# Optimization experiments

Hardware: AMD Instinct MI355X
Metric: run time of the kernel (lower is better)

The kernel has to match this reference:

```python
import jax, jax.numpy as jnp
import numpy as np

VOCAB, EMBED, BLOCK, HEADS, LAYERS = 96, 192, 128, 6, 6
HS = EMBED // HEADS  # 32
B, T = 256, 128
EPS = 1e-5


def layer_norm(x, g, b):
    m = jnp.mean(x, axis=-1, keepdims=True)
    v = jnp.mean(jnp.square(x - m), axis=-1, keepdims=True)
    return (x - m) * jax.lax.rsqrt(v + EPS) * g + b


def setup_inputs() -> dict:
    key = jax.random.key(0)
    ks = jax.random.split(key, 20)
    s = 0.02
    return {
        "index": jax.random.randint(ks[0], (B, T), 0, VOCAB),
        "targets": jax.random.randint(ks[1], (B, T), 0, VOCAB),
        "tok_emb": jax.random.normal(ks[2], (VOCAB, EMBED), jnp.float32) * s,
        "pos_emb": jax.random.normal(ks[3], (BLOCK, EMBED), jnp.float32) * s,
        "ln1_g": jnp.ones((LAYERS, EMBED), jnp.float32),
        "ln1_b": jnp.zeros((LAYERS, EMBED), jnp.float32),
        "ln2_g": jnp.ones((LAYERS, EMBED), jnp.float32),
        "ln2_b": jnp.zeros((LAYERS, EMBED), jnp.float32),
        "Wq": jax.random.normal(ks[4], (LAYERS, HEADS, EMBED, HS), jnp.float32) * s,
        "Wk": jax.random.normal(ks[5], (LAYERS, HEADS, EMBED, HS), jnp.float32) * s,
        "Wv": jax.random.normal(ks[6], (LAYERS, HEADS, EMBED, HS), jnp.float32) * s,
        "W1": jax.random.normal(ks[7], (LAYERS, EMBED, 4 * EMBED), jnp.float32) * s,
        "b1": jnp.zeros((LAYERS, 4 * EMBED), jnp.float32),
        "W2": jax.random.normal(ks[8], (LAYERS, 4 * EMBED, EMBED), jnp.float32) * s,
        "b2": jnp.zeros((LAYERS, EMBED), jnp.float32),
        "fn_g": jnp.ones((EMBED,), jnp.float32),
        "fn_b": jnp.zeros((EMBED,), jnp.float32),
        "Wf": jax.random.normal(ks[9], (EMBED, VOCAB), jnp.float32) * s,
        "bf": jnp.zeros((VOCAB,), jnp.float32),
    }


def reference(index, targets, tok_emb, pos_emb, ln1_g, ln1_b, ln2_g, ln2_b,
              Wq, Wk, Wv, W1, b1, W2, b2, fn_g, fn_b, Wf, bf):
    t = index.shape[1]
    x = tok_emb[index] + pos_emb[:t]                      # [B,T,E]
    causal = jnp.tril(jnp.ones((t, t), bool))             # [T,T]
    for l in range(LAYERS):
        n1 = layer_norm(x, ln1_g[l], ln1_b[l])
        # --- per-head attention, computed but (faithfully) unused by the block ---
        q = jnp.einsum('bte,hes->bhts', n1, Wq[l])
        k = jnp.einsum('bte,hes->bhts', n1, Wk[l])
        v = jnp.einsum('bte,hes->bhts', n1, Wv[l])
        w = jnp.einsum('bhts,bhus->bhtu', q, k) * (EMBED ** -0.5)  # note: scaled by embed, as in source
        w = jnp.where(causal, w, -jnp.inf)
        wei = jax.nn.softmax(w, axis=-1)
        _attn_out = jnp.einsum('bhtu,bhus->bhts', wei, v)  # dead in original forward
        # --- actual block output: FFN on ln2(ln1(x)), no residual ---
        n2 = layer_norm(n1, ln2_g[l], ln2_b[l])
        h = jnp.maximum(jnp.einsum('bte,ef->btf', n2, W1[l]) + b1[l], 0.0)
        x = jnp.einsum('btf,fe->bte', h, W2[l]) + b2[l]
    x = layer_norm(x, fn_g, fn_b)
    logits = jnp.einsum('bte,ev->btv', x, Wf) + bf        # [B,T,V]
    pred = logits.reshape(-1, VOCAB)                      # [B*T,V]
    tgt = targets.reshape(-1)
    logp = jax.nn.log_softmax(pred, axis=-1)
    loss = -jnp.mean(jnp.take_along_axis(logp, tgt[:, None], axis=1)[:, 0])
    return pred, loss
```

## Files before the change

kernel.cpp:

```cpp
#include <hip/hip_runtime.h>

typedef __attribute__((ext_vector_type(4))) float f32x4;
typedef __attribute__((ext_vector_type(8))) short short8;
typedef unsigned short ushort_t;
typedef unsigned int uint_t;

#define R_  32768
#define L_  6
#define EPS_ 1e-5f

#define NW_ 884736

__device__ __forceinline__ ushort_t f2bf(float f) {
    uint_t i = __builtin_bit_cast(uint_t, f);
    uint_t r = (i + 0x7fffu + ((i >> 16) & 1u)) >> 16;
    return (ushort_t)r;
}
__device__ __forceinline__ uint_t cvtpk(float a, float b) {
    uint_t r;
    asm("v_cvt_pk_bf16_f32 %0, %1, %2" : "=v"(r) : "v"(a), "v"(b));
    return r;
}

__global__ void wconv_k(const float* __restrict__ W1, const float* __restrict__ W2,
                        const float* __restrict__ Wf,
                        ushort_t* __restrict__ w1s, ushort_t* __restrict__ w2s,
                        ushort_t* __restrict__ wfr)
{
    int i = blockIdx.x * 256 + threadIdx.x;
    if (i < NW_) {
        int j = i & 7, li = (i >> 3) & 63, q = i >> 9;
        int kc = q % 6; q /= 6;
        int ft = q % 6; q /= 6;
        int wv = q & 3; q >>= 2;
        int half = q & 1; int l = q >> 1;
        int f = half * 384 + wv * 96 + ft * 16 + (li & 15);
        int k = kc * 32 + ((li >> 4) << 3) + j;
        w1s[i] = f2bf(W1[((size_t)l * 192 + k) * 768 + f]);
        return;
    }
    i -= NW_;
    if (i < NW_) {
        int j = i & 7, li = (i >> 3) & 63, q = i >> 9;
        int kc2 = q % 12; q /= 12;
        int ei = q % 3; q /= 3;
        int wv = q & 3; q >>= 2;
        int half = q & 1; int l = q >> 1;
        int e = (wv + 4 * ei) * 16 + (li & 15);
        int k = half * 384 + kc2 * 32 + ((li >> 4) << 3) + j;
        w2s[i] = f2bf(W2[((size_t)l * 768 + k) * 192 + e]);
        return;
    }
    i -= NW_;
    if (i < 36 * 512) {
        int j = i & 7, li = (i >> 3) & 63, q = i >> 9;
        int kc = q % 6, vt = q / 6;
        int v = vt * 16 + (li & 15);
        int k = kc * 32 + ((li >> 4) << 3) + j;
        wfr[i] = f2bf(Wf[(size_t)k * 96 + v]);
    }
}

__global__ __launch_bounds__(256, 2) void net_k(
    const int* __restrict__ idxp, const int* __restrict__ tgp,
    const float* __restrict__ tok, const float* __restrict__ pos,
    const float* __restrict__ ln1g, const float* __restrict__ ln1b,
    const float* __restrict__ ln2g, const float* __restrict__ ln2b,
    const float* __restrict__ b1g, const float* __restrict__ b2g,
    const float* __restrict__ fng, const float* __restrict__ fnb,
    const float* __restrict__ bfb,
    const ushort_t* __restrict__ w1s, const ushort_t* __restrict__ w2s,
    const ushort_t* __restrict__ wfr,
    float* __restrict__ pred, float* __restrict__ partial)
{
    __shared__ __align__(16) ushort_t xb[6 * 4 * 512];
    __shared__ __align__(16) ushort_t hbl[12 * 4 * 512];
    __shared__ __align__(16) float lnS1[64][4], lnQ1[64][4];
    __shared__ __align__(16) float lnS2[64][4], lnQ2[64][4];
    __shared__ float lsred[4];

    const int tid = threadIdx.x, lane = tid & 63, w = tid >> 6;
    const int c = lane & 15, g = lane >> 4;
    const int row0 = blockIdx.x * 64;

    f32x4 xac[3][4];

#pragma unroll
    for (int rg = 0; rg < 4; ++rg) {
        int row = row0 + rg * 16 + c;
        int id = idxp[row];
        int tt = row & 127;
#pragma unroll
        for (int i = 0; i < 3; ++i) {
            int e0 = (w + 4 * i) * 16 + g * 4;
            float4 a = *(const float4*)(tok + (size_t)id * 192 + e0);
            float4 b = *(const float4*)(pos + (size_t)tt * 192 + e0);
            xac[i][rg][0] = a.x + b.x; xac[i][rg][1] = a.y + b.y;
            xac[i][rg][2] = a.z + b.z; xac[i][rg][3] = a.w + b.w;
        }
    }

#pragma unroll 1
    for (int l = 0; l < L_; ++l) {
#pragma unroll
        for (int rg = 0; rg < 4; ++rg) {
            float s = 0.f, sq = 0.f;
#pragma unroll
            for (int i = 0; i < 3; ++i)
#pragma unroll
                for (int r = 0; r < 4; ++r) { float v = xac[i][rg][r]; s += v; sq += v * v; }
            s += __shfl_xor(s, 16); sq += __shfl_xor(sq, 16);
            s += __shfl_xor(s, 32); sq += __shfl_xor(sq, 32);
            if (g == 0) { lnS1[rg * 16 + c][w] = s; lnQ1[rg * 16 + c][w] = sq; }
        }
        __syncthreads();
#pragma unroll
        for (int rg = 0; rg < 4; ++rg) {
            float4 S = *(const float4*)lnS1[rg * 16 + c];
            float4 Q = *(const float4*)lnQ1[rg * 16 + c];
            float mu = (S.x + S.y + S.z + S.w) * (1.f / 192.f);
            float var = (Q.x + Q.y + Q.z + Q.w) * (1.f / 192.f) - mu * mu;
            float ri = rsqrtf(var + EPS_);
            float s2 = 0.f, q2 = 0.f;
#pragma unroll
            for (int i = 0; i < 3; ++i) {
                int e0 = (w + 4 * i) * 16 + g * 4;
                float4 gg = *(const float4*)(ln1g + l * 192 + e0);
                float4 bb = *(const float4*)(ln1b + l * 192 + e0);
                float n0 = (xac[i][rg][0] - mu) * ri * gg.x + bb.x;
                float n1 = (xac[i][rg][1] - mu) * ri * gg.y + bb.y;
                float n2 = (xac[i][rg][2] - mu) * ri * gg.z + bb.z;
                float n3 = (xac[i][rg][3] - mu) * ri * gg.w + bb.w;
                xac[i][rg][0] = n0; xac[i][rg][1] = n1; xac[i][rg][2] = n2; xac[i][rg][3] = n3;
                s2 += n0 + n1 + n2 + n3;
                q2 += n0 * n0 + n1 * n1 + n2 * n2 + n3 * n3;
            }
            s2 += __shfl_xor(s2, 16); q2 += __shfl_xor(q2, 16);
            s2 += __shfl_xor(s2, 32); q2 += __shfl_xor(q2, 32);
            if (g == 0) { lnS2[rg * 16 + c][w] = s2; lnQ2[rg * 16 + c][w] = q2; }
        }
        __syncthreads();
#pragma unroll
        for (int rg = 0; rg < 4; ++rg) {
            float4 S = *(const float4*)lnS2[rg * 16 + c];
            float4 Q = *(const float4*)lnQ2[rg * 16 + c];
            float mu = (S.x + S.y + S.z + S.w) * (1.f / 192.f);
            float var = (Q.x + Q.y + Q.z + Q.w) * (1.f / 192.f) - mu * mu;
            float ri = rsqrtf(var + EPS_);
#pragma unroll
            for (int i = 0; i < 3; ++i) {
                int et = w + 4 * i;
                int e0 = et * 16 + g * 4;
                float4 gg = *(const float4*)(ln2g + l * 192 + e0);
                float4 bb = *(const float4*)(ln2b + l * 192 + e0);
                float y0 = (xac[i][rg][0] - mu) * ri * gg.x + bb.x;
                float y1 = (xac[i][rg][1] - mu) * ri * gg.y + bb.y;
                float y2 = (xac[i][rg][2] - mu) * ri * gg.z + bb.z;
                float y3 = (xac[i][rg][3] - mu) * ri * gg.w + bb.w;
                uint_t d0 = cvtpk(y0, y1), d1 = cvtpk(y2, y3);
                int kc = et >> 1, floc = ((et & 1) << 4) + g * 4;
                int us = (kc * 4 + rg) * 512 + ((floc >> 3) * 16 + c) * 8 + (floc & 7);
                *(uint2*)(xb + us) = make_uint2(d0, d1);
                float4 b2v = *(const float4*)(b2g + l * 192 + e0);
                xac[i][rg][0] = b2v.x; xac[i][rg][1] = b2v.y;
                xac[i][rg][2] = b2v.z; xac[i][rg][3] = b2v.w;
            }
        }
        __syncthreads();

#pragma unroll 1
        for (int half = 0; half < 2; ++half) {
            const ushort_t* w1p = w1s + ((size_t)((l * 2 + half) * 4 + w) * 36) * 512 + lane * 8;
#pragma unroll
            for (int fth = 0; fth < 2; ++fth) {
                short8 wa[18];
#pragma unroll
                for (int q = 0; q < 18; ++q) wa[q] = *(const short8*)(w1p + (fth * 18 + q) * 512);
                float4 bbv[3];
#pragma unroll
                for (int f3 = 0; f3 < 3; ++f3)
                    bbv[f3] = *(const float4*)(b1g + l * 768 + half * 384 + w * 96 + (fth * 3 + f3) * 16 + g * 4);
#pragma unroll
                for (int rg = 0; rg < 4; ++rg) {
                    short8 xbf[6];
#pragma unroll
                    for (int kc = 0; kc < 6; ++kc)
                        xbf[kc] = *(const short8*)(xb + (kc * 4 + rg) * 512 + lane * 8);
#pragma unroll
                    for (int f3 = 0; f3 < 3; ++f3) {
                        f32x4 acc;
                        acc[0] = bbv[f3].x; acc[1] = bbv[f3].y;
                        acc[2] = bbv[f3].z; acc[3] = bbv[f3].w;
                        __builtin_amdgcn_s_setprio(1);
#pragma unroll
                        for (int kc = 0; kc < 6; ++kc)
                            acc = __builtin_amdgcn_mfma_f32_16x16x32_bf16(wa[f3 * 6 + kc], xbf[kc], acc, 0, 0, 0);
                        __builtin_amdgcn_s_setprio(0);
                        float y0 = fmaxf(acc[0], 0.f);
                        float y1 = fmaxf(acc[1], 0.f);
                        float y2 = fmaxf(acc[2], 0.f);
                        float y3 = fmaxf(acc[3], 0.f);
                        uint_t d0 = cvtpk(y0, y1), d1 = cvtpk(y2, y3);
                        int ft = fth * 3 + f3;
                        int kc2 = w * 3 + (ft >> 1);
                        int floc = ((ft & 1) << 4) + g * 4;
                        int us = (kc2 * 4 + rg) * 512 + ((floc >> 3) * 16 + c) * 8 + (floc & 7);
                        *(uint2*)(hbl + us) = make_uint2(d0, d1);
                    }
                }
            }
            __syncthreads();

            const ushort_t* w2p = w2s + ((size_t)((l * 2 + half) * 4 + w) * 36) * 512 + lane * 8;
#pragma unroll
            for (int kh = 0; kh < 2; ++kh) {
                short8 wr[18];
#pragma unroll
                for (int ei = 0; ei < 3; ++ei)
#pragma unroll
                    for (int k6 = 0; k6 < 6; ++k6)
                        wr[ei * 6 + k6] = *(const short8*)(w2p + (ei * 12 + kh * 6 + k6) * 512);
#pragma unroll
                for (int rg = 0; rg < 4; ++rg) {
                    short8 hbf[6];
#pragma unroll
                    for (int k6 = 0; k6 < 6; ++k6)
                        hbf[k6] = *(const short8*)(hbl + ((kh * 6 + k6) * 4 + rg) * 512 + lane * 8);
                    __builtin_amdgcn_s_setprio(1);
#pragma unroll
                    for (int ei = 0; ei < 3; ++ei)
#pragma unroll
                        for (int k6 = 0; k6 < 6; ++k6)
                            xac[ei][rg] = __builtin_amdgcn_mfma_f32_16x16x32_bf16(wr[ei * 6 + k6], hbf[k6], xac[ei][rg], 0, 0, 0);
                    __builtin_amdgcn_s_setprio(0);
                }
            }
            if (half == 0) __syncthreads();
        }
    }

#pragma unroll
    for (int rg = 0; rg < 4; ++rg) {
        float s = 0.f, sq = 0.f;
#pragma unroll
        for (int i = 0; i < 3; ++i)
#pragma unroll
            for (int r = 0; r < 4; ++r) { float v = xac[i][rg][r]; s += v; sq += v * v; }
        s += __shfl_xor(s, 16); sq += __shfl_xor(sq, 16);
        s += __shfl_xor(s, 32); sq += __shfl_xor(sq, 32);
        if (g == 0) { lnS1[rg * 16 + c][w] = s; lnQ1[rg * 16 + c][w] = sq; }
    }
    __syncthreads();
#pragma unroll
    for (int rg = 0; rg < 4; ++rg) {
        float4 S = *(const float4*)lnS1[rg * 16 + c];
        float4 Q = *(const float4*)lnQ1[rg * 16 + c];
        float mu = (S.x + S.y + S.z + S.w) * (1.f / 192.f);
        float var = (Q.x + Q.y + Q.z + Q.w) * (1.f / 192.f) - mu * mu;
        float ri = rsqrtf(var + EPS_);
#pragma unroll
        for (int i = 0; i < 3; ++i) {
            int et = w + 4 * i;
            int e0 = et * 16 + g * 4;
            float4 gg = *(const float4*)(fng + e0);
            float4 bb = *(const float4*)(fnb + e0);
            float y0 = (xac[i][rg][0] - mu) * ri * gg.x + bb.x;
            float y1 = (xac[i][rg][1] - mu) * ri * gg.y + bb.y;
            float y2 = (xac[i][rg][2] - mu) * ri * gg.z + bb.z;
            float y3 = (xac[i][rg][3] - mu) * ri * gg.w + bb.w;
            uint_t d0 = cvtpk(y0, y1), d1 = cvtpk(y2, y3);
            int kc = et >> 1, floc = ((et & 1) << 4) + g * 4;
            int us = (kc * 4 + rg) * 512 + ((floc >> 3) * 16 + c) * 8 + (floc & 7);
            *(uint2*)(xb + us) = make_uint2(d0, d1);
        }
    }
    __syncthreads();

    short8 wfh[36];
    {
        const ushort_t* wfp = wfr + lane * 8;
#pragma unroll
        for (int q = 0; q < 36; ++q) wfh[q] = *(const short8*)(wfp + q * 512);
    }
    short8 xbf[6];
#pragma unroll
    for (int kc = 0; kc < 6; ++kc)
        xbf[kc] = *(const short8*)(xb + (kc * 4 + w) * 512 + lane * 8);
    f32x4 av[6] = {};
    __builtin_amdgcn_s_setprio(1);
#pragma unroll
    for (int vt = 0; vt < 6; ++vt)
#pragma unroll
        for (int kc = 0; kc < 6; ++kc)
            av[vt] = __builtin_amdgcn_mfma_f32_16x16x32_bf16(wfh[vt * 6 + kc], xbf[kc], av[vt], 0, 0, 0);
    __builtin_amdgcn_s_setprio(0);

    float vv[6][4];
#pragma unroll
    for (int vt = 0; vt < 6; ++vt) {
        float4 bb = *(const float4*)(bfb + vt * 16 + g * 4);
        vv[vt][0] = av[vt][0] + bb.x;
        vv[vt][1] = av[vt][1] + bb.y;
        vv[vt][2] = av[vt][2] + bb.z;
        vv[vt][3] = av[vt][3] + bb.w;
    }
    float mx = -1e30f;
#pragma unroll
    for (int vt = 0; vt < 6; ++vt)
#pragma unroll
        for (int r = 0; r < 4; ++r) mx = fmaxf(mx, vv[vt][r]);
    mx = fmaxf(mx, __shfl_xor(mx, 16));
    mx = fmaxf(mx, __shfl_xor(mx, 32));
    float se = 0.f;
#pragma unroll
    for (int vt = 0; vt < 6; ++vt)
#pragma unroll
        for (int r = 0; r < 4; ++r) se += expf(vv[vt][r] - mx);
    se += __shfl_xor(se, 16);
    se += __shfl_xor(se, 32);
    float lse = logf(se) + mx;
    int myrow = row0 + w * 16 + c;
    int tgt = tgp[myrow];
    float lsum = 0.f;
#pragma unroll
    for (int vt = 0; vt < 6; ++vt)
#pragma unroll
        for (int r = 0; r < 4; ++r)
            if (tgt == vt * 16 + g * 4 + r) lsum += lse - vv[vt][r];
#pragma unroll
    for (int vt = 0; vt < 6; ++vt) {
        float4 o;
        o.x = vv[vt][0]; o.y = vv[vt][1]; o.z = vv[vt][2]; o.w = vv[vt][3];
        *(float4*)(pred + (size_t)myrow * 96 + vt * 16 + g * 4) = o;
    }
#pragma unroll
    for (int m = 1; m < 64; m <<= 1) lsum += __shfl_xor(lsum, m);
    if (lane == 0) lsred[w] = lsum;
    __syncthreads();
    if (tid == 0) partial[blockIdx.x] = lsred[0] + lsred[1] + lsred[2] + lsred[3];
}

__global__ void lossred_k(const float* __restrict__ partial, float* __restrict__ out)
{
    __shared__ double sd[256];
    int t = threadIdx.x;
    sd[t] = (double)partial[t] + (double)partial[t + 256];
    __syncthreads();
    for (int s = 128; s > 0; s >>= 1) {
        if (t < s) sd[t] += sd[t + s];
        __syncthreads();
    }
    if (t == 0) out[0] = (float)(sd[0] / (double)R_);
}

extern "C" void kernel_launch(void* const* d_in, const int* in_sizes, int n_in,
                              void* d_out, int out_size, void* d_ws, size_t ws_size,
                              hipStream_t stream)
{
    (void)in_sizes; (void)n_in; (void)out_size; (void)ws_size;
    const int*   index   = (const int*)  d_in[0];
    const int*   targets = (const int*)  d_in[1];
    const float* tok     = (const float*)d_in[2];
    const float* pos     = (const float*)d_in[3];
    const float* ln1g    = (const float*)d_in[4];
    const float* ln1b    = (const float*)d_in[5];
    const float* ln2g    = (const float*)d_in[6];
    const float* ln2b    = (const float*)d_in[7];
    const float* W1      = (const float*)d_in[11];
    const float* b1      = (const float*)d_in[12];
    const float* W2      = (const float*)d_in[13];
    const float* b2      = (const float*)d_in[14];
    const float* fng     = (const float*)d_in[15];
    const float* fnb     = (const float*)d_in[16];
    const float* Wf      = (const float*)d_in[17];
    const float* bfv     = (const float*)d_in[18];

    ushort_t* w1s = (ushort_t*)d_ws;
    ushort_t* w2s = w1s + NW_;
    ushort_t* wfr = w2s + NW_;
    float* partial = (float*)(wfr + 36 * 512);
    float* pred  = (float*)d_out;
    float* lossp = pred + (size_t)R_ * 96;

    const int nconv = 2 * NW_ + 36 * 512;
    wconv_k<<<nconv / 256, 256, 0, stream>>>(W1, W2, Wf, w1s, w2s, wfr);
    net_k<<<512, 256, 0, stream>>>(index, targets, tok, pos, ln1g, ln1b, ln2g, ln2b,
                                   b1, b2, fng, fnb, bfv, w1s, w2s, wfr, pred, partial);
    lossred_k<<<1, 256, 0, stream>>>(partial, lossp);
}
```

Baseline: 148.6 us.

## Split FFN hidden dim into quarters to shrink LDS and raise occupancy

The FFN hidden dimension is now processed in four chunks of 192 instead of two halves of 384. This halves the hidden-activation LDS buffer and cuts per-wave weight register arrays, so launch bounds can ask for 3 blocks per SM instead of 2. The W1/W2 pre-swizzle layout is rewritten to match, and the final projection loads its weights in two groups to lower register pressure. The cost is twice as many barriers per layer and smaller weight tiles between syncs, which gives less latency hiding per block.

```diff
diff --git a/kernel.cpp b/kernel.cpp
--- a/kernel.cpp
+++ b/kernel.cpp
@@ -31,10 +31,10 @@
     if (i < NW_) {
         int j = i & 7, li = (i >> 3) & 63, q = i >> 9;
         int kc = q % 6; q /= 6;
-        int ft = q % 6; q /= 6;
+        int ft = q % 3; q /= 3;
         int wv = q & 3; q >>= 2;
-        int half = q & 1; int l = q >> 1;
-        int f = half * 384 + wv * 96 + ft * 16 + (li & 15);
+        int qt = q & 3; int l = q >> 2;
+        int f = qt * 192 + wv * 48 + ft * 16 + (li & 15);
         int k = kc * 32 + ((li >> 4) << 3) + j;
         w1s[i] = f2bf(W1[((size_t)l * 192 + k) * 768 + f]);
         return;
@@ -42,12 +42,12 @@
     i -= NW_;
     if (i < NW_) {
         int j = i & 7, li = (i >> 3) & 63, q = i >> 9;
-        int kc2 = q % 12; q /= 12;
+        int kc2 = q % 6; q /= 6;
         int ei = q % 3; q /= 3;
         int wv = q & 3; q >>= 2;
-        int half = q & 1; int l = q >> 1;
+        int qt = q & 3; int l = q >> 2;
         int e = (wv + 4 * ei) * 16 + (li & 15);
-        int k = half * 384 + kc2 * 32 + ((li >> 4) << 3) + j;
+        int k = qt * 192 + kc2 * 32 + ((li >> 4) << 3) + j;
         w2s[i] = f2bf(W2[((size_t)l * 768 + k) * 192 + e]);
         return;
     }
@@ -61,7 +61,7 @@
     }
 }
 
-__global__ __launch_bounds__(256, 2) void net_k(
+__global__ __launch_bounds__(256, 3) void net_k(
     const int* __restrict__ idxp, const int* __restrict__ tgp,
     const float* __restrict__ tok, const float* __restrict__ pos,
     const float* __restrict__ ln1g, const float* __restrict__ ln1b,
@@ -74,7 +74,7 @@
     float* __restrict__ pred, float* __restrict__ partial)
 {
     __shared__ __align__(16) ushort_t xb[6 * 4 * 512];
-    __shared__ __align__(16) ushort_t hbl[12 * 4 * 512];
+    __shared__ __align__(16) ushort_t hbl[6 * 4 * 512];
     __shared__ __align__(16) float lnS1[64][4], lnQ1[64][4];
     __shared__ __align__(16) float lnS2[64][4], lnQ2[64][4];
     __shared__ float lsred[4];
@@ -169,73 +169,64 @@
         __syncthreads();
 
 #pragma unroll 1
-        for (int half = 0; half < 2; ++half) {
-            const ushort_t* w1p = w1s + ((size_t)((l * 2 + half) * 4 + w) * 36) * 512 + lane * 8;
-#pragma unroll
-            for (int fth = 0; fth < 2; ++fth) {
-                short8 wa[18];
-#pragma unroll
-                for (int q = 0; q < 18; ++q) wa[q] = *(const short8*)(w1p + (fth * 18 + q) * 512);
-                float4 bbv[3];
-#pragma unroll
-                for (int f3 = 0; f3 < 3; ++f3)
-                    bbv[f3] = *(const float4*)(b1g + l * 768 + half * 384 + w * 96 + (fth * 3 + f3) * 16 + g * 4);
-#pragma unroll
-                for (int rg = 0; rg < 4; ++rg) {
-                    short8 xbf[6];
+        for (int qt = 0; qt < 4; ++qt) {
+            const ushort_t* w1p = w1s + ((size_t)((l * 4 + qt) * 4 + w) * 18) * 512 + lane * 8;
+            short8 wa[18];
+#pragma unroll
+            for (int q = 0; q < 18; ++q) wa[q] = *(const short8*)(w1p + q * 512);
+            float4 bbv[3];
+#pragma unroll
+            for (int f3 = 0; f3 < 3; ++f3)
+                bbv[f3] = *(const float4*)(b1g + l * 768 + qt * 192 + w * 48 + f3 * 16 + g * 4);
+#pragma unroll
+            for (int rg = 0; rg < 4; ++rg) {
+                short8 xbf[6];
+#pragma unroll
+                for (int kc = 0; kc < 6; ++kc)
+                    xbf[kc] = *(const short8*)(xb + (kc * 4 + rg) * 512 + lane * 8);
+#pragma unroll
+                for (int ft = 0; ft < 3; ++ft) {
+                    f32x4 acc;
+                    acc[0] = bbv[ft].x; acc[1] = bbv[ft].y;
+                    acc[2] = bbv[ft].z; acc[3] = bbv[ft].w;
+                    __builtin_amdgcn_s_setprio(1);
 #pragma unroll
                     for (int kc = 0; kc < 6; ++kc)
-                        xbf[kc] = *(const short8*)(xb + (kc * 4 + rg) * 512 + lane * 8);
-#pragma unroll
-                    for (int f3 = 0; f3 < 3; ++f3) {
-                        f32x4 acc;
-                        acc[0] = bbv[f3].x; acc[1] = bbv[f3].y;
-                        acc[2] = bbv[f3].z; acc[3] = bbv[f3].w;
-                        __builtin_amdgcn_s_setprio(1);
-#pragma unroll
-                        for (int kc = 0; kc < 6; ++kc)
-                            acc = __builtin_amdgcn_mfma_f32_16x16x32_bf16(wa[f3 * 6 + kc], xbf[kc], acc, 0, 0, 0);
-                        __builtin_amdgcn_s_setprio(0);
-                        float y0 = fmaxf(acc[0], 0.f);
-                        float y1 = fmaxf(acc[1], 0.f);
-                        float y2 = fmaxf(acc[2], 0.f);
-                        float y3 = fmaxf(acc[3], 0.f);
-                        uint_t d0 = cvtpk(y0, y1), d1 = cvtpk(y2, y3);
-                        int ft = fth * 3 + f3;
-                        int kc2 = w * 3 + (ft >> 1);
-                        int floc = ((ft & 1) << 4) + g * 4;
-                        int us = (kc2 * 4 + rg) * 512 + ((floc >> 3) * 16 + c) * 8 + (floc & 7);
-                        *(uint2*)(hbl + us) = make_uint2(d0, d1);
-                    }
+                        acc = __builtin_amdgcn_mfma_f32_16x16x32_bf16(wa[ft * 6 + kc], xbf[kc], acc, 0, 0, 0);
+                    __builtin_amdgcn_s_setprio(0);
+                    float y0 = fmaxf(acc[0], 0.f);
+                    float y1 = fmaxf(acc[1], 0.f);
+                    float y2 = fmaxf(acc[2], 0.f);
+                    float y3 = fmaxf(acc[3], 0.f);
+                    uint_t d0 = cvtpk(y0, y1), d1 = cvtpk(y2, y3);
+                    int fg = w * 48 + ft * 16;
+                    int kc2 = fg >> 5;
+                    int floc = (fg & 31) + g * 4;
+                    int us = (kc2 * 4 + rg) * 512 + ((floc >> 3) * 16 + c) * 8 + (floc & 7);
+                    *(uint2*)(hbl + us) = make_uint2(d0, d1);
                 }
             }
             __syncthreads();
 
-            const ushort_t* w2p = w2s + ((size_t)((l * 2 + half) * 4 + w) * 36) * 512 + lane * 8;
-#pragma unroll
-            for (int kh = 0; kh < 2; ++kh) {
-                short8 wr[18];
+            const ushort_t* w2p = w2s + ((size_t)((l * 4 + qt) * 4 + w) * 18) * 512 + lane * 8;
+            short8 wr[18];
+#pragma unroll
+            for (int q = 0; q < 18; ++q) wr[q] = *(const short8*)(w2p + q * 512);
+#pragma unroll
+            for (int rg = 0; rg < 4; ++rg) {
+                short8 hbf[6];
+#pragma unroll
+                for (int k6 = 0; k6 < 6; ++k6)
+                    hbf[k6] = *(const short8*)(hbl + (k6 * 4 + rg) * 512 + lane * 8);
+                __builtin_amdgcn_s_setprio(1);
 #pragma unroll
                 for (int ei = 0; ei < 3; ++ei)
 #pragma unroll
                     for (int k6 = 0; k6 < 6; ++k6)
-                        wr[ei * 6 + k6] = *(const short8*)(w2p + (ei * 12 + kh * 6 + k6) * 512);
-#pragma unroll
-                for (int rg = 0; rg < 4; ++rg) {
-                    short8 hbf[6];
-#pragma unroll
-                    for (int k6 = 0; k6 < 6; ++k6)
-                        hbf[k6] = *(const short8*)(hbl + ((kh * 6 + k6) * 4 + rg) * 512 + lane * 8);
-                    __builtin_amdgcn_s_setprio(1);
-#pragma unroll
-                    for (int ei = 0; ei < 3; ++ei)
-#pragma unroll
-                        for (int k6 = 0; k6 < 6; ++k6)
-                            xac[ei][rg] = __builtin_amdgcn_mfma_f32_16x16x32_bf16(wr[ei * 6 + k6], hbf[k6], xac[ei][rg], 0, 0, 0);
-                    __builtin_amdgcn_s_setprio(0);
-                }
+                        xac[ei][rg] = __builtin_amdgcn_mfma_f32_16x16x32_bf16(wr[ei * 6 + k6], hbf[k6], xac[ei][rg], 0, 0, 0);
+                __builtin_amdgcn_s_setprio(0);
             }
-            if (half == 0) __syncthreads();
+            if (qt < 3) __syncthreads();
         }
     }
 
@@ -276,24 +267,28 @@
     }
     __syncthreads();
 
-    short8 wfh[36];
-    {
-        const ushort_t* wfp = wfr + lane * 8;
-#pragma unroll
-        for (int q = 0; q < 36; ++q) wfh[q] = *(const short8*)(wfp + q * 512);
-    }
     short8 xbf[6];
 #pragma unroll
     for (int kc = 0; kc < 6; ++kc)
         xbf[kc] = *(const short8*)(xb + (kc * 4 + w) * 512 + lane * 8);
-    f32x4 av[6] = {};
-    __builtin_amdgcn_s_setprio(1);
-#pragma unroll
-    for (int vt = 0; vt < 6; ++vt)
-#pragma unroll
-        for (int kc = 0; kc < 6; ++kc)
-            av[vt] = __builtin_amdgcn_mfma_f32_16x16x32_bf16(wfh[vt * 6 + kc], xbf[kc], av[vt], 0, 0, 0);
-    __builtin_amdgcn_s_setprio(0);
+    f32x4 av[6];
+#pragma unroll
+    for (int grp = 0; grp < 2; ++grp) {
+        short8 wfh[18];
+        const ushort_t* wfp = wfr + (size_t)grp * 18 * 512 + lane * 8;
+#pragma unroll
+        for (int q = 0; q < 18; ++q) wfh[q] = *(const short8*)(wfp + q * 512);
+        __builtin_amdgcn_s_setprio(1);
+#pragma unroll
+        for (int vt3 = 0; vt3 < 3; ++vt3) {
+            f32x4 acc = {};
+#pragma unroll
+            for (int kc = 0; kc < 6; ++kc)
+                acc = __builtin_amdgcn_mfma_f32_16x16x32_bf16(wfh[vt3 * 6 + kc], xbf[kc], acc, 0, 0, 0);
+            av[grp * 3 + vt3] = acc;
+        }
+        __builtin_amdgcn_s_setprio(0);
+    }
 
     float vv[6][4];
 #pragma unroll
```

After: 208.1 us. 40.1% more time.
